# Kernel optimization log

Hardware: AMD Instinct MI355X
Metric: run time of the kernel (lower is better)

The kernel has to match this reference:

```python
import jax, jax.numpy as jnp
import numpy as np

B, LAT, FRAME, HID, E, GH = 4096, 64, 512, 1024, 8, 128
IN1 = LAT + FRAME      # 576, fc1/gate input
IN2 = LAT + HID        # 1088, fc2/fc3 input
OUT = FRAME            # 512, num_future_frames * frame_size


def setup_inputs() -> dict:
    key = jax.random.key(0)
    ks = jax.random.split(key, 16)
    s = lambda fan_in: 1.0 / np.sqrt(fan_in)
    inp = {
        "z": jax.random.normal(ks[0], (B, LAT), jnp.float32),
        "c": jax.random.normal(ks[1], (B, FRAME), jnp.float32),
        # expert-mixed layers: weight [E, in, out], bias [E, out]
        "w0": jax.random.uniform(ks[2], (E, IN1, HID), jnp.float32, -s(IN1), s(IN1)),
        "b0": jax.random.uniform(ks[3], (E, HID), jnp.float32, -s(IN1), s(IN1)),
        "w1": jax.random.uniform(ks[4], (E, IN2, HID), jnp.float32, -s(IN2), s(IN2)),
        "b1": jax.random.uniform(ks[5], (E, HID), jnp.float32, -s(IN2), s(IN2)),
        "w2": jax.random.uniform(ks[6], (E, IN2, OUT), jnp.float32, -s(IN2), s(IN2)),
        "b2": jax.random.uniform(ks[7], (E, OUT), jnp.float32, -s(IN2), s(IN2)),
        # gate MLP
        "gw1": jax.random.uniform(ks[8], (IN1, GH), jnp.float32, -s(IN1), s(IN1)),
        "gb1": jax.random.uniform(ks[9], (GH,), jnp.float32, -s(IN1), s(IN1)),
        "gw2": jax.random.uniform(ks[10], (GH, GH), jnp.float32, -s(GH), s(GH)),
        "gb2": jax.random.uniform(ks[11], (GH,), jnp.float32, -s(GH), s(GH)),
        "gw3": jax.random.uniform(ks[12], (GH, E), jnp.float32, -s(GH), s(GH)),
        "gb3": jax.random.uniform(ks[13], (E,), jnp.float32, -s(GH), s(GH)),
    }
    return inp


def _mixed_layer(coef, x, w, b):
    # per-expert projection then softmax-weighted mix: same math as
    # baddbmm(coef@b, x, (coef@flat(w)).view(B,in,out)) in the original.
    ye = jnp.einsum('bi,eio->beo', x, w)          # [B, E, out]
    return jnp.einsum('be,beo->bo', coef, ye) + coef @ b


def reference(z, c, w0, b0, w1, b1, w2, b2, gw1, gb1, gw2, gb2, gw3, gb3):
    x0 = jnp.concatenate([z, c], axis=1)           # [B, IN1]
    h = jax.nn.elu(x0 @ gw1 + gb1)
    h = jax.nn.elu(h @ gw2 + gb2)
    coef = jax.nn.softmax(h @ gw3 + gb3, axis=1)   # [B, E]

    out = jax.nn.elu(_mixed_layer(coef, x0, w0, b0))
    out = jax.nn.elu(_mixed_layer(coef, jnp.concatenate([z, out], axis=1), w1, b1))
    out = _mixed_layer(coef, jnp.concatenate([z, out], axis=1), w2, b2)
    return out
```

## Files before the change

### kernel.cpp

```cpp
#include <hip/hip_runtime.h>
#include <cstdint>
#include <cstddef>

#define B_    4096
#define LAT   64
#define FRAME 512
#define HID   1024
#define NE    8
#define GH    128
#define IN1   576
#define IN2   1088

typedef __bf16 bf16x8 __attribute__((ext_vector_type(8)));
typedef float  f32x4  __attribute__((ext_vector_type(4)));

__device__ inline unsigned short f2bf(float f) {
  union { float f; uint32_t u; } c; c.f = f;
  uint32_t u = c.u;
  return (unsigned short)((u + 0x7FFFu + ((u >> 16) & 1u)) >> 16);
}

__device__ inline void async16(const void* g, void* l) {
  __builtin_amdgcn_global_load_lds(
      (__attribute__((address_space(1))) void*)(void*)g,
      (__attribute__((address_space(3))) void*)l, 16, 0, 0);
}

__global__ __launch_bounds__(256) void gate_kernel(
    const float* __restrict__ z, const float* __restrict__ c,
    const float* __restrict__ gw1, const float* __restrict__ gb1,
    const float* __restrict__ gw2, const float* __restrict__ gb2,
    const float* __restrict__ gw3, const float* __restrict__ gb3,
    float* __restrict__ coef)
{
  __shared__ float xs[16][IN1 + 1];
  __shared__ float hs[16][GH + 1];
  __shared__ float h2s[16][GH + 1];
  __shared__ float ls[16][NE];
  const int tid = threadIdx.x;
  const int r0 = blockIdx.x * 16;

  for (int i = tid; i < 16 * IN1; i += 256) {
    int r = i / IN1, j = i - r * IN1;
    xs[r][j] = (j < LAT) ? z[(size_t)(r0 + r) * LAT + j]
                         : c[(size_t)(r0 + r) * FRAME + (j - LAT)];
  }
  __syncthreads();
  {
    const int col = tid & 127, rbase = tid >> 7;
    float acc[8];
    for (int q = 0; q < 8; ++q) acc[q] = gb1[col];
    for (int i = 0; i < IN1; ++i) {
      float w = gw1[(size_t)i * GH + col];
      for (int q = 0; q < 8; ++q) acc[q] += w * xs[rbase + 2 * q][i];
    }
    for (int q = 0; q < 8; ++q) {
      float v = acc[q];
      hs[rbase + 2 * q][col] = v > 0.f ? v : expm1f(v);
    }
  }
  __syncthreads();
  {
    const int col = tid & 127, rbase = tid >> 7;
    float acc[8];
    for (int q = 0; q < 8; ++q) acc[q] = gb2[col];
    for (int i = 0; i < GH; ++i) {
      float w = gw2[(size_t)i * GH + col];
      for (int q = 0; q < 8; ++q) acc[q] += w * hs[rbase + 2 * q][i];
    }
    for (int q = 0; q < 8; ++q) {
      float v = acc[q];
      h2s[rbase + 2 * q][col] = v > 0.f ? v : expm1f(v);
    }
  }
  __syncthreads();
  if (tid < 128) {
    int r = tid >> 3, e = tid & 7;
    float acc = gb3[e];
    for (int i = 0; i < GH; ++i) acc += h2s[r][i] * gw3[(size_t)i * NE + e];
    ls[r][e] = acc;
  }
  __syncthreads();
  if (tid < 16) {
    int r = tid;
    float m = ls[r][0];
    for (int e = 1; e < NE; ++e) m = fmaxf(m, ls[r][e]);
    float ex[NE], s = 0.f;
    for (int e = 0; e < NE; ++e) { ex[e] = expf(ls[r][e] - m); s += ex[e]; }
    float inv = 1.f / s;
    for (int e = 0; e < NE; ++e) coef[(size_t)(r0 + r) * NE + e] = ex[e] * inv;
  }
}


__global__ __launch_bounds__(256) void transpose_cast_flat(
    const float* __restrict__ in, unsigned short* __restrict__ out, int K, int N)
{
  __shared__ float t[32][33];
  const int e = blockIdx.z;
  const int n0 = blockIdx.x * 32, k0 = blockIdx.y * 32;
  const float* ine = in + (size_t)e * K * N;
  const int tx = threadIdx.x, ty = threadIdx.y;
  for (int it = 0; it < 4; ++it)
    t[ty + it * 8][tx] = ine[(size_t)(k0 + ty + it * 8) * N + n0 + tx];
  __syncthreads();
  for (int it = 0; it < 4; ++it)
    out[(size_t)(n0 + ty + it * 8) * (NE * K) + (size_t)e * K + k0 + tx] =
        f2bf(t[tx][ty + it * 8]);
}

__global__ __launch_bounds__(256) void build_xp1(
    const float* __restrict__ z, const float* __restrict__ c,
    const float* __restrict__ coef, unsigned short* __restrict__ xp)
{
  int idx = blockIdx.x * 256 + threadIdx.x;
  int b = idx / IN1, j = idx - b * IN1;
  float v = (j < LAT) ? z[(size_t)b * LAT + j] : c[(size_t)b * FRAME + (j - LAT)];
  const float* cf = coef + (size_t)b * NE;
  unsigned short* row = xp + (size_t)b * (NE * IN1) + j;
  #pragma unroll
  for (int e = 0; e < NE; ++e) row[(size_t)e * IN1] = f2bf(cf[e] * v);
}

template<int KP, int NOUT, int KSTEPS>
__global__ __launch_bounds__(256, 3) void gemm_bt(
    const unsigned short* __restrict__ Xp,
    const unsigned short* __restrict__ Wt,
    float* __restrict__ part)
{
  __shared__ __align__(16) unsigned short As[128 * 64];
  __shared__ __align__(16) unsigned short Bs[128 * 64];
  const int tid = threadIdx.x;
  const int wave = tid >> 6, lane = tid & 63;
  const int wm = wave & 1, wn = wave >> 1;
  const int quad = lane >> 4, l16 = lane & 15;
  const int bm0 = blockIdx.x * 128, bn0 = blockIdx.y * 128;
  const int kbase = blockIdx.z * (KSTEPS * 64);

  f32x4 acc[4][4];
  #pragma unroll
  for (int mi = 0; mi < 4; ++mi)
    #pragma unroll
    for (int ni = 0; ni < 4; ++ni)
      #pragma unroll
      for (int r = 0; r < 4; ++r) acc[mi][ni][r] = 0.f;

  const int srow  = wave * 8 + (lane >> 3);
  const int skoff = (((lane & 7) ^ ((lane >> 3) & 7)) * 8);

  for (int ki = 0; ki < KSTEPS; ++ki) {
    const int k0 = kbase + ki * 64;
    #pragma unroll
    for (int it = 0; it < 4; ++it) {
      async16(Xp + (size_t)(bm0 + it * 32 + srow) * KP + k0 + skoff,
              &As[it * 2048 + wave * 512]);
      async16(Wt + (size_t)(bn0 + it * 32 + srow) * KP + k0 + skoff,
              &Bs[it * 2048 + wave * 512]);
    }
    __syncthreads();
    #pragma unroll
    for (int ks = 0; ks < 64; ks += 32) {
      bf16x8 af[4], bv[4];
      #pragma unroll
      for (int mi = 0; mi < 4; ++mi) {
        const int r = wm * 64 + mi * 16 + l16;
        const int g = (ks / 8 + quad) ^ (r & 7);
        af[mi] = *(const bf16x8*)&As[r * 64 + g * 8];
      }
      #pragma unroll
      for (int ni = 0; ni < 4; ++ni) {
        const int r = wn * 64 + ni * 16 + l16;
        const int g = (ks / 8 + quad) ^ (r & 7);
        bv[ni] = *(const bf16x8*)&Bs[r * 64 + g * 8];
      }
      #pragma unroll
      for (int mi = 0; mi < 4; ++mi)
        #pragma unroll
        for (int ni = 0; ni < 4; ++ni)
          acc[mi][ni] = __builtin_amdgcn_mfma_f32_16x16x32_bf16(
              af[mi], bv[ni], acc[mi][ni], 0, 0, 0);
    }
    __syncthreads();
  }

  float* po = part + (size_t)blockIdx.z * B_ * NOUT;
  #pragma unroll
  for (int mi = 0; mi < 4; ++mi)
    #pragma unroll
    for (int r = 0; r < 4; ++r) {
      const int m_loc = wm * 64 + mi * 16 + quad * 4 + r;
      #pragma unroll
      for (int ni = 0; ni < 4; ++ni) {
        const int n_loc = wn * 64 + ni * 16 + l16;
        po[(size_t)(bm0 + m_loc) * NOUT + bn0 + n_loc] = acc[mi][ni][r];
      }
    }
}

template<int KSPLIT>
__global__ __launch_bounds__(256) void expand_xp(
    const float* __restrict__ part,
    const float* __restrict__ bias,
    const float* __restrict__ z,
    const float* __restrict__ coef,
    unsigned short* __restrict__ xp)
{
  int idx = blockIdx.x * 256 + threadIdx.x;
  int b = idx / IN2, j = idx - b * IN2;
  const float* cf = coef + (size_t)b * NE;
  float cl[NE];
  #pragma unroll
  for (int e = 0; e < NE; ++e) cl[e] = cf[e];
  float v;
  if (j < LAT) {
    v = z[(size_t)b * LAT + j];
  } else {
    int h = j - LAT;
    v = 0.f;
    #pragma unroll
    for (int s = 0; s < KSPLIT; ++s)
      v += part[(size_t)s * B_ * HID + (size_t)b * HID + h];
    #pragma unroll
    for (int e = 0; e < NE; ++e) v += cl[e] * bias[(size_t)e * HID + h];
    v = v > 0.f ? v : expm1f(v);
  }
  unsigned short* row = xp + (size_t)b * (NE * IN2) + j;
  #pragma unroll
  for (int e = 0; e < NE; ++e) row[(size_t)e * IN2] = f2bf(cl[e] * v);
}

template<int KSPLIT>
__global__ __launch_bounds__(256) void final_out(
    const float* __restrict__ part,
    const float* __restrict__ bias2,
    const float* __restrict__ coef,
    float* __restrict__ out)
{
  int idx = blockIdx.x * 256 + threadIdx.x;
  int b = idx / FRAME, n = idx - b * FRAME;
  float v = 0.f;
  #pragma unroll
  for (int s = 0; s < KSPLIT; ++s)
    v += part[(size_t)s * B_ * FRAME + idx];
  const float* cf = coef + (size_t)b * NE;
  #pragma unroll
  for (int e = 0; e < NE; ++e) v += cf[e] * bias2[(size_t)e * FRAME + n];
  out[idx] = v;
}


__global__ __launch_bounds__(256) void build_x(
    const float* __restrict__ z, const float* __restrict__ c,
    unsigned short* __restrict__ x1, unsigned short* __restrict__ x2,
    unsigned short* __restrict__ x3)
{
  int idx = blockIdx.x * 256 + threadIdx.x;
  if (idx >= B_ * IN1) return;
  int b = idx / IN1, j = idx - b * IN1;
  float v = (j < LAT) ? z[(size_t)b * LAT + j] : c[(size_t)b * FRAME + (j - LAT)];
  unsigned short h = f2bf(v);
  x1[(size_t)b * IN1 + j] = h;
  if (j < LAT) {
    x2[(size_t)b * IN2 + j] = h;
    x3[(size_t)b * IN2 + j] = h;
  }
}

__global__ __launch_bounds__(256) void transpose_cast(
    const float* __restrict__ in, unsigned short* __restrict__ out, int K, int N)
{
  __shared__ float t[32][33];
  const int e = blockIdx.z;
  const int n0 = blockIdx.x * 32, k0 = blockIdx.y * 32;
  const float* ine = in + (size_t)e * K * N;
  unsigned short* oute = out + (size_t)e * N * K;
  const int tx = threadIdx.x, ty = threadIdx.y;
  for (int it = 0; it < 4; ++it)
    t[ty + it * 8][tx] = ine[(size_t)(k0 + ty + it * 8) * N + n0 + tx];
  __syncthreads();
  for (int it = 0; it < 4; ++it)
    oute[(size_t)(n0 + ty + it * 8) * K + k0 + tx] = f2bf(t[tx][ty + it * 8]);
}

template<int KDIM, int NOUT, int ECNT, bool ELU_ACT, bool FINAL>
__global__ __launch_bounds__(256) void gemm_moe(
    const unsigned short* __restrict__ X,
    const unsigned short* __restrict__ Wt,
    const float* __restrict__ bias,
    const float* __restrict__ coef,
    unsigned short* __restrict__ next_x,
    float* __restrict__ outf)
{
  __shared__ __align__(16) unsigned short As[128 * 64];
  __shared__ __align__(16) unsigned short Bs[64 * 64];
  __shared__ float coefS[128 * NE];
  __shared__ float biasS[NE * 64];

  const int tid = threadIdx.x;
  const int wave = tid >> 6, lane = tid & 63;
  const int wm = wave & 1, wn = wave >> 1;
  const int quad = lane >> 4, l16 = lane & 15;
  const int bm0 = blockIdx.x * 128, bn0 = blockIdx.y * 64;
  const int ebase = FINAL ? blockIdx.z * ECNT : 0;

  for (int i = tid; i < 128 * NE; i += 256)
    coefS[i] = coef[(size_t)(bm0 + (i >> 3)) * NE + (i & 7)];
  for (int i = tid; i < NE * 64; i += 256)
    biasS[i] = bias[(size_t)(i >> 6) * NOUT + bn0 + (i & 63)];

  f32x4 accT[4][2];
  #pragma unroll
  for (int mi = 0; mi < 4; ++mi)
    #pragma unroll
    for (int ni = 0; ni < 2; ++ni)
      #pragma unroll
      for (int r = 0; r < 4; ++r) accT[mi][ni][r] = 0.f;

  const int srow  = wave * 8 + (lane >> 3);
  const int skoff = (((lane & 7) ^ ((lane >> 3) & 7)) * 8);

  for (int e = 0; e < ECNT; ++e) {
    const size_t eoff = (size_t)(ebase + e) * NOUT * KDIM;
    f32x4 accE[4][2];
    #pragma unroll
    for (int mi = 0; mi < 4; ++mi)
      #pragma unroll
      for (int ni = 0; ni < 2; ++ni)
        #pragma unroll
        for (int r = 0; r < 4; ++r) accE[mi][ni][r] = 0.f;

    for (int k0 = 0; k0 < KDIM; k0 += 64) {
      #pragma unroll
      for (int it = 0; it < 4; ++it)
        async16(X + (size_t)(bm0 + it * 32 + srow) * KDIM + k0 + skoff,
                &As[it * 2048 + wave * 512]);
      #pragma unroll
      for (int it = 0; it < 2; ++it)
        async16(Wt + eoff + (size_t)(bn0 + it * 32 + srow) * KDIM + k0 + skoff,
                &Bs[it * 2048 + wave * 512]);
      __syncthreads();
      #pragma unroll
      for (int ks = 0; ks < 64; ks += 32) {
        bf16x8 af[4], bv[2];
        #pragma unroll
        for (int mi = 0; mi < 4; ++mi) {
          const int r = wm * 64 + mi * 16 + l16;
          const int g = (ks / 8 + quad) ^ (r & 7);
          af[mi] = *(const bf16x8*)&As[r * 64 + g * 8];
        }
        #pragma unroll
        for (int ni = 0; ni < 2; ++ni) {
          const int r = wn * 32 + ni * 16 + l16;
          const int g = (ks / 8 + quad) ^ (r & 7);
          bv[ni] = *(const bf16x8*)&Bs[r * 64 + g * 8];
        }
        #pragma unroll
        for (int mi = 0; mi < 4; ++mi)
          #pragma unroll
          for (int ni = 0; ni < 2; ++ni)
            accE[mi][ni] = __builtin_amdgcn_mfma_f32_16x16x32_bf16(
                af[mi], bv[ni], accE[mi][ni], 0, 0, 0);
      }
      __syncthreads();
    }
    #pragma unroll
    for (int mi = 0; mi < 4; ++mi) {
      float cf[4];
      #pragma unroll
      for (int r = 0; r < 4; ++r)
        cf[r] = coefS[(wm * 64 + mi * 16 + quad * 4 + r) * NE + ebase + e];
      #pragma unroll
      for (int ni = 0; ni < 2; ++ni)
        #pragma unroll
        for (int r = 0; r < 4; ++r)
          accT[mi][ni][r] += cf[r] * accE[mi][ni][r];
    }
  }

  #pragma unroll
  for (int mi = 0; mi < 4; ++mi) {
    #pragma unroll
    for (int r = 0; r < 4; ++r) {
      const int m_loc = wm * 64 + mi * 16 + quad * 4 + r;
      const size_t grow = (size_t)(bm0 + m_loc);
      #pragma unroll
      for (int ni = 0; ni < 2; ++ni) {
        const int n_loc = wn * 32 + ni * 16 + l16;
        float v = accT[mi][ni][r];
        if (!FINAL || blockIdx.z == 0) {
          #pragma unroll
          for (int e = 0; e < NE; ++e)
            v += coefS[m_loc * NE + e] * biasS[e * 64 + n_loc];
        }
        if (ELU_ACT) v = v > 0.f ? v : expm1f(v);
        if (FINAL) atomicAdd(&outf[grow * NOUT + bn0 + n_loc], v);
        else       next_x[grow * IN2 + LAT + bn0 + n_loc] = f2bf(v);
      }
    }
  }
}


extern "C" void kernel_launch(void* const* d_in, const int* in_sizes, int n_in,
                              void* d_out, int out_size, void* d_ws, size_t ws_size,
                              hipStream_t stream)
{
  const float* z   = (const float*)d_in[0];
  const float* c   = (const float*)d_in[1];
  const float* w0  = (const float*)d_in[2];
  const float* b0  = (const float*)d_in[3];
  const float* w1  = (const float*)d_in[4];
  const float* b1  = (const float*)d_in[5];
  const float* w2  = (const float*)d_in[6];
  const float* b2  = (const float*)d_in[7];
  const float* gw1 = (const float*)d_in[8];
  const float* gb1 = (const float*)d_in[9];
  const float* gw2 = (const float*)d_in[10];
  const float* gb2 = (const float*)d_in[11];
  const float* gw3 = (const float*)d_in[12];
  const float* gb3 = (const float*)d_in[13];
  float* out = (float*)d_out;
  char* ws = (char*)d_ws;

  const size_t OFF_XP   = 131072;
  const size_t OFF_WT   = 71434240;
  const size_t OFF_PART = 89260032;
  const size_t NEED     = 122814464;

  float* coef = (float*)(ws + 0);

  if (ws_size >= NEED) {
    unsigned short* Xp   = (unsigned short*)(ws + OFF_XP);
    unsigned short* Wt   = (unsigned short*)(ws + OFF_WT);
    float*          part = (float*)         (ws + OFF_PART);

    gate_kernel<<<B_ / 16, 256, 0, stream>>>(z, c, gw1, gb1, gw2, gb2, gw3, gb3, coef);
    build_xp1<<<(B_ * IN1) / 256, 256, 0, stream>>>(z, c, coef, Xp);

    transpose_cast_flat<<<dim3(HID / 32, IN1 / 32, NE), dim3(32, 8), 0, stream>>>(w0, Wt, IN1, HID);
    gemm_bt<NE * IN1, HID, 36><<<dim3(32, 8, 2), 256, 0, stream>>>(Xp, Wt, part);
    expand_xp<2><<<(B_ * IN2) / 256, 256, 0, stream>>>(part, b0, z, coef, Xp);

    transpose_cast_flat<<<dim3(HID / 32, IN2 / 32, NE), dim3(32, 8), 0, stream>>>(w1, Wt, IN2, HID);
    gemm_bt<NE * IN2, HID, 68><<<dim3(32, 8, 2), 256, 0, stream>>>(Xp, Wt, part);
    expand_xp<2><<<(B_ * IN2) / 256, 256, 0, stream>>>(part, b1, z, coef, Xp);

    transpose_cast_flat<<<dim3(FRAME / 32, IN2 / 32, NE), dim3(32, 8), 0, stream>>>(w2, Wt, IN2, FRAME);
    gemm_bt<NE * IN2, FRAME, 34><<<dim3(32, 4, 4), 256, 0, stream>>>(Xp, Wt, part);
    final_out<4><<<(B_ * FRAME) / 256, 256, 0, stream>>>(part, b2, coef, out);
    return;
  }

  unsigned short* x1  = (unsigned short*)(ws + 131072);
  unsigned short* x2  = (unsigned short*)(ws + 4849664);
  unsigned short* x3  = (unsigned short*)(ws + 13762560);
  unsigned short* Wt0 = (unsigned short*)(ws + 22675456);
  unsigned short* Wt1 = (unsigned short*)(ws + 32112640);
  unsigned short* Wt2 = (unsigned short*)(ws + 49938432);

  hipMemsetAsync(out, 0, (size_t)B_ * FRAME * sizeof(float), stream);
  gate_kernel<<<B_ / 16, 256, 0, stream>>>(z, c, gw1, gb1, gw2, gb2, gw3, gb3, coef);
  build_x<<<(B_ * IN1) / 256, 256, 0, stream>>>(z, c, x1, x2, x3);
  transpose_cast<<<dim3(HID / 32, IN1 / 32, NE), dim3(32, 8), 0, stream>>>(w0, Wt0, IN1, HID);
  transpose_cast<<<dim3(HID / 32, IN2 / 32, NE), dim3(32, 8), 0, stream>>>(w1, Wt1, IN2, HID);
  transpose_cast<<<dim3(FRAME / 32, IN2 / 32, NE), dim3(32, 8), 0, stream>>>(w2, Wt2, IN2, FRAME);
  gemm_moe<IN1, HID, NE, true, false><<<dim3(32, 16), 256, 0, stream>>>(x1, Wt0, b0, coef, x2, nullptr);
  gemm_moe<IN2, HID, NE, true, false><<<dim3(32, 16), 256, 0, stream>>>(x2, Wt1, b1, coef, x3, nullptr);
  gemm_moe<IN2, FRAME, 4, false, true><<<dim3(32, 8, 2), 256, 0, stream>>>(x3, Wt2, b2, coef, nullptr, out);
}
```

Measured before the change: 420.6 us.

## Move gate MLP to fp16 MFMA and switch split-K GEMMs to atomic accumulation

Replaces the scalar FP32 gate MLP with an MFMA-based kernel that processes 128 rows per block, using fp16-transposed gate weights prepared by a new kernel. The split-K partial buffers are replaced with atomicAdd into a single zeroed buffer, and split-K factors are doubled (2→4, 4→8) so more blocks run in parallel. Launch bounds occupancy rises from 3 to 4 blocks, and the fallback path for small workspaces is deleted. The trade-offs are lower gate precision (fp16 inputs), extra memsets, atomic contention, and dependence on a large workspace.

```diff
diff --git a/kernel.cpp b/kernel.cpp
--- a/kernel.cpp
+++ b/kernel.cpp
@@ -12,6 +12,7 @@
 #define IN2   1088
 
 typedef __bf16 bf16x8 __attribute__((ext_vector_type(8)));
+typedef _Float16 half8 __attribute__((ext_vector_type(8)));
 typedef float  f32x4  __attribute__((ext_vector_type(4)));
 
 __device__ inline unsigned short f2bf(float f) {
@@ -26,72 +27,145 @@
       (__attribute__((address_space(3))) void*)l, 16, 0, 0);
 }
 
-__global__ __launch_bounds__(256) void gate_kernel(
+__device__ inline float elu(float v) { return v > 0.f ? v : expm1f(v); }
+
+__global__ __launch_bounds__(256) void prep_gatew(
+    const float* __restrict__ gw1, const float* __restrict__ gw2,
+    _Float16* __restrict__ gw1T, _Float16* __restrict__ gw2T)
+{
+  __shared__ float t[32][33];
+  const int tx = threadIdx.x, ty = threadIdx.y;
+  int bx = blockIdx.x;
+  const float* in; _Float16* out; int K, N, kt, nt;
+  if (bx < 72) { in = gw1; out = gw1T; K = 576; N = 128; kt = bx >> 2; nt = bx & 3; }
+  else { bx -= 72; in = gw2; out = gw2T; K = 128; N = 128; kt = bx >> 2; nt = bx & 3; }
+  const int k0 = kt * 32, n0 = nt * 32;
+  for (int it = 0; it < 4; ++it)
+    t[ty + it * 8][tx] = in[(size_t)(k0 + ty + it * 8) * N + n0 + tx];
+  __syncthreads();
+  for (int it = 0; it < 4; ++it)
+    out[(size_t)(n0 + ty + it * 8) * K + k0 + tx] = (_Float16)t[tx][ty + it * 8];
+}
+
+__global__ __launch_bounds__(256) void gate_mfma(
     const float* __restrict__ z, const float* __restrict__ c,
-    const float* __restrict__ gw1, const float* __restrict__ gb1,
-    const float* __restrict__ gw2, const float* __restrict__ gb2,
+    const _Float16* __restrict__ gw1T,
+    const _Float16* __restrict__ gw2T,
+    const float* __restrict__ gb1, const float* __restrict__ gb2,
     const float* __restrict__ gw3, const float* __restrict__ gb3,
     float* __restrict__ coef)
 {
-  __shared__ float xs[16][IN1 + 1];
-  __shared__ float hs[16][GH + 1];
-  __shared__ float h2s[16][GH + 1];
-  __shared__ float ls[16][NE];
+  __shared__ _Float16 h_lds[128][136];
+  __shared__ float    h2_lds[128][129];
+  __shared__ float    gw3s[128 * 8];
   const int tid = threadIdx.x;
-  const int r0 = blockIdx.x * 16;
-
-  for (int i = tid; i < 16 * IN1; i += 256) {
-    int r = i / IN1, j = i - r * IN1;
-    xs[r][j] = (j < LAT) ? z[(size_t)(r0 + r) * LAT + j]
-                         : c[(size_t)(r0 + r) * FRAME + (j - LAT)];
-  }
+  const int wave = tid >> 6, lane = tid & 63;
+  const int quad = lane >> 4, l16 = lane & 15;
+  const int r0 = blockIdx.x * 128;
+
+  for (int i = tid; i < 128 * 8; i += 256) gw3s[i] = gw3[i];
+
+  f32x4 acc[2][8];
+  #pragma unroll
+  for (int mt = 0; mt < 2; ++mt)
+    #pragma unroll
+    for (int nt = 0; nt < 8; ++nt)
+      #pragma unroll
+      for (int r = 0; r < 4; ++r) acc[mt][nt][r] = 0.f;
+
+  #pragma unroll 2
+  for (int s = 0; s < 18; ++s) {
+    const int k0 = s * 32;
+    half8 af[2];
+    #pragma unroll
+    for (int mt = 0; mt < 2; ++mt) {
+      const size_t row = r0 + wave * 32 + mt * 16 + l16;
+      const float* src = (k0 < LAT) ? z + row * LAT + k0 + quad * 8
+                                    : c + row * FRAME + (k0 - LAT) + quad * 8;
+      f32x4 lo = *(const f32x4*)src, hi = *(const f32x4*)(src + 4);
+      #pragma unroll
+      for (int j = 0; j < 4; ++j) { af[mt][j] = (_Float16)lo[j]; af[mt][j + 4] = (_Float16)hi[j]; }
+    }
+    half8 bfr[8];
+    #pragma unroll
+    for (int nt = 0; nt < 8; ++nt)
+      bfr[nt] = *(const half8*)(gw1T + (size_t)(nt * 16 + l16) * 576 + k0 + quad * 8);
+    #pragma unroll
+    for (int mt = 0; mt < 2; ++mt)
+      #pragma unroll
+      for (int nt = 0; nt < 8; ++nt)
+        acc[mt][nt] = __builtin_amdgcn_mfma_f32_16x16x32_f16(af[mt], bfr[nt], acc[mt][nt], 0, 0, 0);
+  }
+  #pragma unroll
+  for (int mt = 0; mt < 2; ++mt)
+    #pragma unroll
+    for (int nt = 0; nt < 8; ++nt)
+      #pragma unroll
+      for (int r = 0; r < 4; ++r) {
+        const int rowl = wave * 32 + mt * 16 + quad * 4 + r;
+        const int col = nt * 16 + l16;
+        h_lds[rowl][col] = (_Float16)elu(acc[mt][nt][r] + gb1[col]);
+      }
   __syncthreads();
+
+  f32x4 acc2[2][8];
+  #pragma unroll
+  for (int mt = 0; mt < 2; ++mt)
+    #pragma unroll
+    for (int nt = 0; nt < 8; ++nt)
+      #pragma unroll
+      for (int r = 0; r < 4; ++r) acc2[mt][nt][r] = 0.f;
+  #pragma unroll
+  for (int s = 0; s < 4; ++s) {
+    const int k0 = s * 32;
+    half8 af[2];
+    #pragma unroll
+    for (int mt = 0; mt < 2; ++mt)
+      af[mt] = *(const half8*)&h_lds[wave * 32 + mt * 16 + l16][k0 + quad * 8];
+    half8 bfr[8];
+    #pragma unroll
+    for (int nt = 0; nt < 8; ++nt)
+      bfr[nt] = *(const half8*)(gw2T + (size_t)(nt * 16 + l16) * 128 + k0 + quad * 8);
+    #pragma unroll
+    for (int mt = 0; mt < 2; ++mt)
+      #pragma unroll
+      for (int nt = 0; nt < 8; ++nt)
+        acc2[mt][nt] = __builtin_amdgcn_mfma_f32_16x16x32_f16(af[mt], bfr[nt], acc2[mt][nt], 0, 0, 0);
+  }
+  #pragma unroll
+  for (int mt = 0; mt < 2; ++mt)
+    #pragma unroll
+    for (int nt = 0; nt < 8; ++nt)
+      #pragma unroll
+      for (int r = 0; r < 4; ++r) {
+        const int rowl = wave * 32 + mt * 16 + quad * 4 + r;
+        const int col = nt * 16 + l16;
+        h2_lds[rowl][col] = elu(acc2[mt][nt][r] + gb2[col]);
+      }
+  __syncthreads();
+
   {
-    const int col = tid & 127, rbase = tid >> 7;
-    float acc[8];
-    for (int q = 0; q < 8; ++q) acc[q] = gb1[col];
-    for (int i = 0; i < IN1; ++i) {
-      float w = gw1[(size_t)i * GH + col];
-      for (int q = 0; q < 8; ++q) acc[q] += w * xs[rbase + 2 * q][i];
-    }
-    for (int q = 0; q < 8; ++q) {
-      float v = acc[q];
-      hs[rbase + 2 * q][col] = v > 0.f ? v : expm1f(v);
-    }
-  }
-  __syncthreads();
-  {
-    const int col = tid & 127, rbase = tid >> 7;
-    float acc[8];
-    for (int q = 0; q < 8; ++q) acc[q] = gb2[col];
-    for (int i = 0; i < GH; ++i) {
-      float w = gw2[(size_t)i * GH + col];
-      for (int q = 0; q < 8; ++q) acc[q] += w * hs[rbase + 2 * q][i];
-    }
-    for (int q = 0; q < 8; ++q) {
-      float v = acc[q];
-      h2s[rbase + 2 * q][col] = v > 0.f ? v : expm1f(v);
-    }
-  }
-  __syncthreads();
-  if (tid < 128) {
-    int r = tid >> 3, e = tid & 7;
-    float acc = gb3[e];
-    for (int i = 0; i < GH; ++i) acc += h2s[r][i] * gw3[(size_t)i * NE + e];
-    ls[r][e] = acc;
-  }
-  __syncthreads();
-  if (tid < 16) {
-    int r = tid;
-    float m = ls[r][0];
-    for (int e = 1; e < NE; ++e) m = fmaxf(m, ls[r][e]);
-    float ex[NE], s = 0.f;
-    for (int e = 0; e < NE; ++e) { ex[e] = expf(ls[r][e] - m); s += ex[e]; }
-    float inv = 1.f / s;
-    for (int e = 0; e < NE; ++e) coef[(size_t)(r0 + r) * NE + e] = ex[e] * inv;
-  }
-}
-
+    const int row = tid >> 1, eh = (tid & 1) * 4;
+    float l4[4];
+    #pragma unroll
+    for (int j = 0; j < 4; ++j) l4[j] = gb3[eh + j];
+    for (int k = 0; k < 128; ++k) {
+      const float hv = h2_lds[row][k];
+      #pragma unroll
+      for (int j = 0; j < 4; ++j) l4[j] += hv * gw3s[k * 8 + eh + j];
+    }
+    float m4 = fmaxf(fmaxf(l4[0], l4[1]), fmaxf(l4[2], l4[3]));
+    const float M = fmaxf(m4, __shfl_xor(m4, 1));
+    float e4[4], s = 0.f;
+    #pragma unroll
+    for (int j = 0; j < 4; ++j) { e4[j] = expf(l4[j] - M); s += e4[j]; }
+    const float inv = 1.f / (s + __shfl_xor(s, 1));
+    f32x4 o;
+    #pragma unroll
+    for (int j = 0; j < 4; ++j) o[j] = e4[j] * inv;
+    *(f32x4*)&coef[(size_t)(r0 + row) * NE + eh] = o;
+  }
+}
 
 __global__ __launch_bounds__(256) void transpose_cast_flat(
     const float* __restrict__ in, unsigned short* __restrict__ out, int K, int N)
@@ -123,7 +197,7 @@
 }
 
 template<int KP, int NOUT, int KSTEPS>
-__global__ __launch_bounds__(256, 3) void gemm_bt(
+__global__ __launch_bounds__(256, 4) void gemm_bt(
     const unsigned short* __restrict__ Xp,
     const unsigned short* __restrict__ Wt,
     float* __restrict__ part)
@@ -183,7 +257,6 @@
     __syncthreads();
   }
 
-  float* po = part + (size_t)blockIdx.z * B_ * NOUT;
   #pragma unroll
   for (int mi = 0; mi < 4; ++mi)
     #pragma unroll
@@ -192,12 +265,11 @@
       #pragma unroll
       for (int ni = 0; ni < 4; ++ni) {
         const int n_loc = wn * 64 + ni * 16 + l16;
-        po[(size_t)(bm0 + m_loc) * NOUT + bn0 + n_loc] = acc[mi][ni][r];
-      }
-    }
-}
-
-template<int KSPLIT>
+        atomicAdd(&part[(size_t)(bm0 + m_loc) * NOUT + bn0 + n_loc], acc[mi][ni][r]);
+      }
+    }
+}
+
 __global__ __launch_bounds__(256) void expand_xp(
     const float* __restrict__ part,
     const float* __restrict__ bias,
@@ -216,20 +288,16 @@
     v = z[(size_t)b * LAT + j];
   } else {
     int h = j - LAT;
-    v = 0.f;
-    #pragma unroll
-    for (int s = 0; s < KSPLIT; ++s)
-      v += part[(size_t)s * B_ * HID + (size_t)b * HID + h];
+    v = part[(size_t)b * HID + h];
     #pragma unroll
     for (int e = 0; e < NE; ++e) v += cl[e] * bias[(size_t)e * HID + h];
-    v = v > 0.f ? v : expm1f(v);
+    v = elu(v);
   }
   unsigned short* row = xp + (size_t)b * (NE * IN2) + j;
   #pragma unroll
   for (int e = 0; e < NE; ++e) row[(size_t)e * IN2] = f2bf(cl[e] * v);
 }
 
-template<int KSPLIT>
 __global__ __launch_bounds__(256) void final_out(
     const float* __restrict__ part,
     const float* __restrict__ bias2,
@@ -238,166 +306,11 @@
 {
   int idx = blockIdx.x * 256 + threadIdx.x;
   int b = idx / FRAME, n = idx - b * FRAME;
-  float v = 0.f;
-  #pragma unroll
-  for (int s = 0; s < KSPLIT; ++s)
-    v += part[(size_t)s * B_ * FRAME + idx];
+  float v = part[idx];
   const float* cf = coef + (size_t)b * NE;
   #pragma unroll
   for (int e = 0; e < NE; ++e) v += cf[e] * bias2[(size_t)e * FRAME + n];
   out[idx] = v;
-}
-
-
-__global__ __launch_bounds__(256) void build_x(
-    const float* __restrict__ z, const float* __restrict__ c,
-    unsigned short* __restrict__ x1, unsigned short* __restrict__ x2,
-    unsigned short* __restrict__ x3)
-{
-  int idx = blockIdx.x * 256 + threadIdx.x;
-  if (idx >= B_ * IN1) return;
-  int b = idx / IN1, j = idx - b * IN1;
-  float v = (j < LAT) ? z[(size_t)b * LAT + j] : c[(size_t)b * FRAME + (j - LAT)];
-  unsigned short h = f2bf(v);
-  x1[(size_t)b * IN1 + j] = h;
-  if (j < LAT) {
-    x2[(size_t)b * IN2 + j] = h;
-    x3[(size_t)b * IN2 + j] = h;
-  }
-}
-
-__global__ __launch_bounds__(256) void transpose_cast(
-    const float* __restrict__ in, unsigned short* __restrict__ out, int K, int N)
-{
-  __shared__ float t[32][33];
-  const int e = blockIdx.z;
-  const int n0 = blockIdx.x * 32, k0 = blockIdx.y * 32;
-  const float* ine = in + (size_t)e * K * N;
-  unsigned short* oute = out + (size_t)e * N * K;
-  const int tx = threadIdx.x, ty = threadIdx.y;
-  for (int it = 0; it < 4; ++it)
-    t[ty + it * 8][tx] = ine[(size_t)(k0 + ty + it * 8) * N + n0 + tx];
-  __syncthreads();
-  for (int it = 0; it < 4; ++it)
-    oute[(size_t)(n0 + ty + it * 8) * K + k0 + tx] = f2bf(t[tx][ty + it * 8]);
-}
-
-template<int KDIM, int NOUT, int ECNT, bool ELU_ACT, bool FINAL>
-__global__ __launch_bounds__(256) void gemm_moe(
-    const unsigned short* __restrict__ X,
-    const unsigned short* __restrict__ Wt,
-    const float* __restrict__ bias,
-    const float* __restrict__ coef,
-    unsigned short* __restrict__ next_x,
-    float* __restrict__ outf)
-{
-  __shared__ __align__(16) unsigned short As[128 * 64];
-  __shared__ __align__(16) unsigned short Bs[64 * 64];
-  __shared__ float coefS[128 * NE];
-  __shared__ float biasS[NE * 64];
-
-  const int tid = threadIdx.x;
-  const int wave = tid >> 6, lane = tid & 63;
-  const int wm = wave & 1, wn = wave >> 1;
-  const int quad = lane >> 4, l16 = lane & 15;
-  const int bm0 = blockIdx.x * 128, bn0 = blockIdx.y * 64;
-  const int ebase = FINAL ? blockIdx.z * ECNT : 0;
-
-  for (int i = tid; i < 128 * NE; i += 256)
-    coefS[i] = coef[(size_t)(bm0 + (i >> 3)) * NE + (i & 7)];
-  for (int i = tid; i < NE * 64; i += 256)
-    biasS[i] = bias[(size_t)(i >> 6) * NOUT + bn0 + (i & 63)];
-
-  f32x4 accT[4][2];
-  #pragma unroll
-  for (int mi = 0; mi < 4; ++mi)
-    #pragma unroll
-    for (int ni = 0; ni < 2; ++ni)
-      #pragma unroll
-      for (int r = 0; r < 4; ++r) accT[mi][ni][r] = 0.f;
-
-  const int srow  = wave * 8 + (lane >> 3);
-  const int skoff = (((lane & 7) ^ ((lane >> 3) & 7)) * 8);
-
-  for (int e = 0; e < ECNT; ++e) {
-    const size_t eoff = (size_t)(ebase + e) * NOUT * KDIM;
-    f32x4 accE[4][2];
-    #pragma unroll
-    for (int mi = 0; mi < 4; ++mi)
-      #pragma unroll
-      for (int ni = 0; ni < 2; ++ni)
-        #pragma unroll
-        for (int r = 0; r < 4; ++r) accE[mi][ni][r] = 0.f;
-
-    for (int k0 = 0; k0 < KDIM; k0 += 64) {
-      #pragma unroll
-      for (int it = 0; it < 4; ++it)
-        async16(X + (size_t)(bm0 + it * 32 + srow) * KDIM + k0 + skoff,
-                &As[it * 2048 + wave * 512]);
-      #pragma unroll
-      for (int it = 0; it < 2; ++it)
-        async16(Wt + eoff + (size_t)(bn0 + it * 32 + srow) * KDIM + k0 + skoff,
-                &Bs[it * 2048 + wave * 512]);
-      __syncthreads();
-      #pragma unroll
-      for (int ks = 0; ks < 64; ks += 32) {
-        bf16x8 af[4], bv[2];
-        #pragma unroll
-        for (int mi = 0; mi < 4; ++mi) {
-          const int r = wm * 64 + mi * 16 + l16;
-          const int g = (ks / 8 + quad) ^ (r & 7);
-          af[mi] = *(const bf16x8*)&As[r * 64 + g * 8];
-        }
-        #pragma unroll
-        for (int ni = 0; ni < 2; ++ni) {
-          const int r = wn * 32 + ni * 16 + l16;
-          const int g = (ks / 8 + quad) ^ (r & 7);
-          bv[ni] = *(const bf16x8*)&Bs[r * 64 + g * 8];
-        }
-        #pragma unroll
-        for (int mi = 0; mi < 4; ++mi)
-          #pragma unroll
-          for (int ni = 0; ni < 2; ++ni)
-            accE[mi][ni] = __builtin_amdgcn_mfma_f32_16x16x32_bf16(
-                af[mi], bv[ni], accE[mi][ni], 0, 0, 0);
-      }
-      __syncthreads();
-    }
-    #pragma unroll
-    for (int mi = 0; mi < 4; ++mi) {
-      float cf[4];
-      #pragma unroll
-      for (int r = 0; r < 4; ++r)
-        cf[r] = coefS[(wm * 64 + mi * 16 + quad * 4 + r) * NE + ebase + e];
-      #pragma unroll
-      for (int ni = 0; ni < 2; ++ni)
-        #pragma unroll
-        for (int r = 0; r < 4; ++r)
-          accT[mi][ni][r] += cf[r] * accE[mi][ni][r];
-    }
-  }
-
-  #pragma unroll
-  for (int mi = 0; mi < 4; ++mi) {
-    #pragma unroll
-    for (int r = 0; r < 4; ++r) {
-      const int m_loc = wm * 64 + mi * 16 + quad * 4 + r;
-      const size_t grow = (size_t)(bm0 + m_loc);
-      #pragma unroll
-      for (int ni = 0; ni < 2; ++ni) {
-        const int n_loc = wn * 32 + ni * 16 + l16;
-        float v = accT[mi][ni][r];
-        if (!FINAL || blockIdx.z == 0) {
-          #pragma unroll
-          for (int e = 0; e < NE; ++e)
-            v += coefS[m_loc * NE + e] * biasS[e * 64 + n_loc];
-        }
-        if (ELU_ACT) v = v > 0.f ? v : expm1f(v);
-        if (FINAL) atomicAdd(&outf[grow * NOUT + bn0 + n_loc], v);
-        else       next_x[grow * IN2 + LAT + bn0 + n_loc] = f2bf(v);
-      }
-    }
-  }
 }
 
 
@@ -422,49 +335,29 @@
   float* out = (float*)d_out;
   char* ws = (char*)d_ws;
 
-  const size_t OFF_XP   = 131072;
-  const size_t OFF_WT   = 71434240;
-  const size_t OFF_PART = 89260032;
-  const size_t NEED     = 122814464;
-
-  float* coef = (float*)(ws + 0);
-
-  if (ws_size >= NEED) {
-    unsigned short* Xp   = (unsigned short*)(ws + OFF_XP);
-    unsigned short* Wt   = (unsigned short*)(ws + OFF_WT);
-    float*          part = (float*)         (ws + OFF_PART);
-
-    gate_kernel<<<B_ / 16, 256, 0, stream>>>(z, c, gw1, gb1, gw2, gb2, gw3, gb3, coef);
-    build_xp1<<<(B_ * IN1) / 256, 256, 0, stream>>>(z, c, coef, Xp);
-
-    transpose_cast_flat<<<dim3(HID / 32, IN1 / 32, NE), dim3(32, 8), 0, stream>>>(w0, Wt, IN1, HID);
-    gemm_bt<NE * IN1, HID, 36><<<dim3(32, 8, 2), 256, 0, stream>>>(Xp, Wt, part);
-    expand_xp<2><<<(B_ * IN2) / 256, 256, 0, stream>>>(part, b0, z, coef, Xp);
-
-    transpose_cast_flat<<<dim3(HID / 32, IN2 / 32, NE), dim3(32, 8), 0, stream>>>(w1, Wt, IN2, HID);
-    gemm_bt<NE * IN2, HID, 68><<<dim3(32, 8, 2), 256, 0, stream>>>(Xp, Wt, part);
-    expand_xp<2><<<(B_ * IN2) / 256, 256, 0, stream>>>(part, b1, z, coef, Xp);
-
-    transpose_cast_flat<<<dim3(FRAME / 32, IN2 / 32, NE), dim3(32, 8), 0, stream>>>(w2, Wt, IN2, FRAME);
-    gemm_bt<NE * IN2, FRAME, 34><<<dim3(32, 4, 4), 256, 0, stream>>>(Xp, Wt, part);
-    final_out<4><<<(B_ * FRAME) / 256, 256, 0, stream>>>(part, b2, coef, out);
-    return;
-  }
-
-  unsigned short* x1  = (unsigned short*)(ws + 131072);
-  unsigned short* x2  = (unsigned short*)(ws + 4849664);
-  unsigned short* x3  = (unsigned short*)(ws + 13762560);
-  unsigned short* Wt0 = (unsigned short*)(ws + 22675456);
-  unsigned short* Wt1 = (unsigned short*)(ws + 32112640);
-  unsigned short* Wt2 = (unsigned short*)(ws + 49938432);
-
-  hipMemsetAsync(out, 0, (size_t)B_ * FRAME * sizeof(float), stream);
-  gate_kernel<<<B_ / 16, 256, 0, stream>>>(z, c, gw1, gb1, gw2, gb2, gw3, gb3, coef);
-  build_x<<<(B_ * IN1) / 256, 256, 0, stream>>>(z, c, x1, x2, x3);
-  transpose_cast<<<dim3(HID / 32, IN1 / 32, NE), dim3(32, 8), 0, stream>>>(w0, Wt0, IN1, HID);
-  transpose_cast<<<dim3(HID / 32, IN2 / 32, NE), dim3(32, 8), 0, stream>>>(w1, Wt1, IN2, HID);
-  transpose_cast<<<dim3(FRAME / 32, IN2 / 32, NE), dim3(32, 8), 0, stream>>>(w2, Wt2, IN2, FRAME);
-  gemm_moe<IN1, HID, NE, true, false><<<dim3(32, 16), 256, 0, stream>>>(x1, Wt0, b0, coef, x2, nullptr);
-  gemm_moe<IN2, HID, NE, true, false><<<dim3(32, 16), 256, 0, stream>>>(x2, Wt1, b1, coef, x3, nullptr);
-  gemm_moe<IN2, FRAME, 4, false, true><<<dim3(32, 8, 2), 256, 0, stream>>>(x3, Wt2, b2, coef, nullptr, out);
-}
+  float*          coef = (float*)         (ws + 0);
+  unsigned short* Xp   = (unsigned short*)(ws + 131072);
+  unsigned short* Wt   = (unsigned short*)(ws + 71434240);
+  float*          part = (float*)         (ws + 89260032);
+  _Float16*       gw1T = (_Float16*)      (ws + 106037248);
+  _Float16*       gw2T = (_Float16*)      (ws + 106184704);
+
+  prep_gatew<<<88, dim3(32, 8), 0, stream>>>(gw1, gw2, gw1T, gw2T);
+  gate_mfma<<<32, 256, 0, stream>>>(z, c, gw1T, gw2T, gb1, gb2, gw3, gb3, coef);
+  build_xp1<<<(B_ * IN1) / 256, 256, 0, stream>>>(z, c, coef, Xp);
+
+  transpose_cast_flat<<<dim3(HID / 32, IN1 / 32, NE), dim3(32, 8), 0, stream>>>(w0, Wt, IN1, HID);
+  hipMemsetAsync(part, 0, (size_t)B_ * HID * 4, stream);
+  gemm_bt<NE * IN1, HID, 18><<<dim3(32, 8, 4), 256, 0, stream>>>(Xp, Wt, part);
+  expand_xp<<<(B_ * IN2) / 256, 256, 0, stream>>>(part, b0, z, coef, Xp);
+
+  transpose_cast_flat<<<dim3(HID / 32, IN2 / 32, NE), dim3(32, 8), 0, stream>>>(w1, Wt, IN2, HID);
+  hipMemsetAsync(part, 0, (size_t)B_ * HID * 4, stream);
+  gemm_bt<NE * IN2, HID, 34><<<dim3(32, 8, 4), 256, 0, stream>>>(Xp, Wt, part);
+  expand_xp<<<(B_ * IN2) / 256, 256, 0, stream>>>(part, b1, z, coef, Xp);
+
+  transpose_cast_flat<<<dim3(FRAME / 32, IN2 / 32, NE), dim3(32, 8), 0, stream>>>(w2, Wt, IN2, FRAME);
+  hipMemsetAsync(part, 0, (size_t)B_ * FRAME * 4, stream);
+  gemm_bt<NE * IN2, FRAME, 17><<<dim3(32, 4, 8), 256, 0, stream>>>(Xp, Wt, part);
+  final_out<<<(B_ * FRAME) / 256, 256, 0, stream>>>(part, b2, coef, out);
+}
```

Result: slower. 520.6 us (+23.8%).
